# Performance work log

Hardware: AMD Instinct MI355X
Metric: run time of the kernel (lower is better)

## Reference

```python
import math
import jax, jax.numpy as jnp
import numpy as np

B, I, D, H, K, MAXI, FF = 2, 1024, 1024, 16, 64, 1024, 4096
DH = D // H
EPS = 1e-5

def _ln(x, g, b):
    m = x.mean(-1, keepdims=True)
    v = ((x - m) ** 2).mean(-1, keepdims=True)
    return (x - m) / jnp.sqrt(v + EPS) * g + b

def setup_inputs() -> dict:
    key = jax.random.key(0)
    ks = jax.random.split(key, 16)
    p = lambda i, sh: (0.02 * jax.random.normal(ks[i], sh)).astype(jnp.float32)
    # clamped relative-position indices: clamp(j - floor(1.0*i), -K, K) + K
    ar = np.arange(MAXI)
    idx = np.clip(ar[None, :] - ar[:, None], -K, K) + K  # [maxI, maxI]
    return {
        'x': jax.random.normal(ks[0], (B, I, D), dtype=jnp.float32),
        'j': jax.random.normal(ks[1], (B, I, D), dtype=jnp.float32),
        'ln1_g': jnp.ones((D,), jnp.float32), 'ln1_b': jnp.zeros((D,), jnp.float32),
        'Wv_w': p(2, (D, D)), 'Wv_b': jnp.zeros((D,), jnp.float32),
        'Wg_w': p(3, (D, D)), 'Wg_b': jnp.zeros((D,), jnp.float32),
        'lnv_g': jnp.ones((D,), jnp.float32), 'lnv_b': jnp.zeros((D,), jnp.float32),
        'Wq1_w': p(4, (D, D)), 'Wq1_b': jnp.zeros((D,), jnp.float32),
        'Wk_w': p(5, (D, D)), 'Wk_b': jnp.zeros((D,), jnp.float32),
        'Wq2_w': p(6, (D, D)), 'Wq2_b': jnp.zeros((D,), jnp.float32),
        'rel_emb': p(7, (2 * K + 1, D)),
        'Wo_w': p(8, (D, D)), 'Wo_b': jnp.zeros((D,), jnp.float32),
        'ln2_g': jnp.ones((D,), jnp.float32), 'ln2_b': jnp.zeros((D,), jnp.float32),
        'ff1_w': p(9, (D, FF)), 'ff1_b': jnp.zeros((FF,), jnp.float32),
        'ff2_w': p(10, (FF, D)), 'ff2_b': jnp.zeros((D,), jnp.float32),
        'indices': jnp.asarray(idx, jnp.int32),
    }

def reference(x, j, ln1_g, ln1_b, Wv_w, Wv_b, Wg_w, Wg_b, lnv_g, lnv_b,
              Wq1_w, Wq1_b, Wk_w, Wk_b, Wq2_w, Wq2_b, rel_emb,
              Wo_w, Wo_b, ln2_g, ln2_b, ff1_w, ff1_b, ff2_w, ff2_b, indices):
    Bv, Iq, _ = x.shape
    res = x
    xn = _ln(x, ln1_g, ln1_b)
    # value / gate streams with gelu activation, layernorm on v only
    v = _ln(jax.nn.gelu(xn @ Wv_w + Wv_b, approximate=False), lnv_g, lnv_b)
    g = jax.nn.gelu(xn @ Wg_w + Wg_b, approximate=False)
    vh = v.reshape(Bv, -1, H, DH)   # [B,J,H,Dh]
    gh = g.reshape(Bv, -1, H, DH)   # [B,I,H,Dh]
    # absolute-position scores: Q1(j) . K(j)^T
    q1 = (j @ Wq1_w + Wq1_b).reshape(Bv, -1, H, DH)
    kh = (j @ Wk_w + Wk_b).reshape(Bv, -1, H, DH)
    aa = jnp.einsum('bihd,bjhd->bhij', q1, kh)  # [B,H,I,J]
    # relative-position scores: Q2(j) . rel_embed^T, gathered by clamped indices
    q2 = (j @ Wq2_w + Wq2_b).reshape(Bv, -1, H, DH)
    rh = rel_emb.reshape(2 * K + 1, H, DH)
    arf = jnp.einsum('bihd,rhd->bhir', q2, rh)  # [B,H,I,2K+1]
    Jk = kh.shape[1]
    idx = jnp.broadcast_to(indices[None, None, :Iq, :Jk], (Bv, H, Iq, Jk))
    ar = jnp.take_along_axis(arf, idx, axis=-1)  # [B,H,I,J]
    a = jax.nn.softmax((aa + ar) / math.sqrt(DH), axis=-1)
    o = jnp.einsum('bhij,bjhd->bihd', a, vh) * gh  # gated attention output
    o = o.reshape(Bv, -1, D) @ Wo_w + Wo_b
    x1 = o + res
    # feed-forward sublayer
    h = jax.nn.relu(_ln(x1, ln2_g, ln2_b) @ ff1_w + ff1_b)
    out = h @ ff2_w + ff2_b + x1
    return (out, a)
```

## Files before the change

### kernel.cpp

```cpp
#include <hip/hip_runtime.h>
#include <hip/hip_bf16.h>
#include <math.h>

#define D_   1024
#define H_   16
#define DH_  64
#define FF_  4096
#define R_   129
#define I_   1024
#define B_   2
#define MROWS 2048
#define QKVLD 3072

typedef __bf16 v8bf16 __attribute__((ext_vector_type(8)));
typedef float f32x4 __attribute__((ext_vector_type(4)));

__device__ __forceinline__ float gelu_f(float x) {
    return 0.5f * x * (1.0f + erff(x * 0.7071067811865476f));
}

__device__ __forceinline__ void ldsld16(const void* g, void* l) {
    __builtin_amdgcn_global_load_lds(
        (const __attribute__((address_space(1))) void*)g,
        (__attribute__((address_space(3))) void*)l, 16, 0, 0);
}

__global__ __launch_bounds__(256) void cvt_bf16(const float* __restrict__ in,
        __hip_bfloat16* __restrict__ out, int n4) {
    int i = blockIdx.x * 256 + threadIdx.x;
    if (i >= n4) return;
    float4 v = reinterpret_cast<const float4*>(in)[i];
    union { __hip_bfloat16 h[4]; uint2 u; } pk;
    pk.h[0] = __float2bfloat16(v.x); pk.h[1] = __float2bfloat16(v.y);
    pk.h[2] = __float2bfloat16(v.z); pk.h[3] = __float2bfloat16(v.w);
    reinterpret_cast<uint2*>(out)[i] = pk.u;
}

__global__ __launch_bounds__(256) void wtrans(const float* __restrict__ W,
        __hip_bfloat16* __restrict__ WT, int K, int N) {
    __shared__ float T[64][65];
    int k0 = blockIdx.y * 64, n0 = blockIdx.x * 64;
    int t = threadIdx.x;
#pragma unroll
    for (int i = 0; i < 16; i++) {
        int e = t + i * 256, r = e >> 6, c = e & 63;
        T[r][c] = W[(size_t)(k0 + r) * N + n0 + c];
    }
    __syncthreads();
#pragma unroll
    for (int i = 0; i < 16; i++) {
        int e = t + i * 256, r = e >> 6, c = e & 63;
        WT[(size_t)(n0 + r) * K + k0 + c] = __float2bfloat16(T[c][r]);
    }
}

__global__ __launch_bounds__(256) void vtrans(const float* __restrict__ v,
        __hip_bfloat16* __restrict__ vt) {
    __shared__ float T[64][65];
    int z = blockIdx.y, b = z >> 4, h = z & 15;
    int j0 = blockIdx.x * 64;
    int t = threadIdx.x;
#pragma unroll
    for (int i = 0; i < 16; i++) {
        int e = t + i * 256, r = e >> 6, c = e & 63;
        T[r][c] = v[(size_t)(b * I_ + j0 + r) * D_ + h * DH_ + c];
    }
    __syncthreads();
#pragma unroll
    for (int i = 0; i < 16; i++) {
        int e = t + i * 256, r = e >> 6, c = e & 63;
        vt[((size_t)z * DH_ + r) * I_ + j0 + c] = __float2bfloat16(T[c][r]);
    }
}

template<int MR, int NWC, int ACT, int RES, int OUTBF>
__global__ __launch_bounds__(256) void gemm_mfma(
        const __hip_bfloat16* __restrict__ A,
        const __hip_bfloat16* __restrict__ Bt,
        const float* __restrict__ bias,
        const float* __restrict__ res,
        void* __restrict__ Cout,
        int N, int Kd, int lda, int ldb, int ldc,
        size_t sAb, size_t sAh, size_t sBb, size_t sBh, size_t sCz) {
    constexpr int NWR = 4 / NWC;
    constexpr int BM = NWR * MR * 16;
    constexpr int BN = NWC * 64;
    __shared__ __align__(16) __hip_bfloat16 As[BM * 64];
    __shared__ __align__(16) __hip_bfloat16 Bs[BN * 64];
    const char* AsB = (const char*)As;
    const char* BsB = (const char*)Bs;
    int z = blockIdx.z;
    const __hip_bfloat16* Ab = A + (size_t)(z >> 4) * sAb + (size_t)(z & 15) * sAh;
    const __hip_bfloat16* Bb = Bt + (size_t)(z >> 4) * sBb + (size_t)(z & 15) * sBh;
    float* Cf = (float*)Cout + (size_t)z * sCz;
    __hip_bfloat16* Cb = (__hip_bfloat16*)Cout + (size_t)z * sCz;
    int m0 = blockIdx.y * BM, n0 = blockIdx.x * BN;
    int t = threadIdx.x;
    int l = t & 63, w = t >> 6;
    int wr = w / NWC, wc = w % NWC;
    int lr = l & 15, kq = l >> 4;
    int rx = lr & 7;

    f32x4 acc[MR][4] = {};

    for (int k0 = 0; k0 < Kd; k0 += 64) {
#pragma unroll
        for (int i = 0; i < BM / 32; i++) {
            int e = t + i * 256;
            int row = e >> 3, sl = e & 7;
            int kb = sl ^ (row & 7);
            ldsld16(Ab + (size_t)(m0 + row) * lda + (k0 + kb * 8), (void*)(AsB + e * 16));
        }
#pragma unroll
        for (int i = 0; i < BN / 32; i++) {
            int e = t + i * 256;
            int row = e >> 3, sl = e & 7;
            int kb = sl ^ (row & 7);
            int nr = n0 + row; if (nr > N - 1) nr = N - 1;
            ldsld16(Bb + (size_t)nr * ldb + (k0 + kb * 8), (void*)(BsB + e * 16));
        }
        __syncthreads();
#pragma unroll
        for (int kc = 0; kc < 2; kc++) {
            int sloff = (((kc << 2) + kq) ^ rx) << 4;
            v8bf16 af[MR], bfr[4];
#pragma unroll
            for (int mr = 0; mr < MR; mr++)
                af[mr] = *(const v8bf16*)(AsB + ((wr * (MR * 16) + mr * 16 + lr) << 7) + sloff);
#pragma unroll
            for (int nc = 0; nc < 4; nc++)
                bfr[nc] = *(const v8bf16*)(BsB + ((wc * 64 + nc * 16 + lr) << 7) + sloff);
#pragma unroll
            for (int mr = 0; mr < MR; mr++)
#pragma unroll
                for (int nc = 0; nc < 4; nc++)
                    acc[mr][nc] = __builtin_amdgcn_mfma_f32_16x16x32_bf16(
                        af[mr], bfr[nc], acc[mr][nc], 0, 0, 0);
        }
        __syncthreads();
    }

#pragma unroll
    for (int mr = 0; mr < MR; mr++) {
        int rbase = m0 + wr * (MR * 16) + mr * 16 + kq * 4;
#pragma unroll
        for (int nc = 0; nc < 4; nc++) {
            int col = n0 + wc * 64 + nc * 16 + lr;
            bool okc = col < N;
            float bv = (bias && okc) ? bias[col] : 0.f;
#pragma unroll
            for (int ri = 0; ri < 4; ri++) {
                int r = rbase + ri;
                float val = acc[mr][nc][ri] + bv;
                if (ACT == 1) val = gelu_f(val);
                if (ACT == 2) val = fmaxf(val, 0.f);
                if (RES) val += res[(size_t)r * ldc + col];
                if (okc) {
                    if (OUTBF) Cb[(size_t)r * ldc + col] = __float2bfloat16(val);
                    else       Cf[(size_t)r * ldc + col] = val;
                }
            }
        }
    }
}

#define FA_AR 0
#define FA_K  16896
#define FA_V  (16896 + 8192)
#define FA_P  (16896 + 16384)
#define SC2   0.1803368801111244f
__global__ __launch_bounds__(256) void flash_attn3(
        const __hip_bfloat16* __restrict__ qkv,
        const __hip_bfloat16* __restrict__ vt,
        const __hip_bfloat16* __restrict__ arfb,
        const __hip_bfloat16* __restrict__ gb,
        float* __restrict__ a_out,
        __hip_bfloat16* __restrict__ obuf) {
    __shared__ __align__(16) char lds[16896 + 8192 * 3];
    __hip_bfloat16* arl = (__hip_bfloat16*)(lds + FA_AR);
    char* kB = lds + FA_K;
    char* vB = lds + FA_V;
    char* pB = lds + FA_P;

    int z = blockIdx.y, b = z >> 4, h = z & 15;
    int i0 = blockIdx.x * 64;
    int t = threadIdx.x, l = t & 63, w = t >> 6;
    int lr = l & 15, kq = l >> 4;

#pragma unroll
    for (int i = 0; i < 2; i++) {
        int e = t + i * 256;
        int row = e >> 3, sl = e & 7;
        int kb = sl ^ (row & 7);
        ldsld16(qkv + (size_t)(b * I_ + i0 + row) * QKVLD + h * DH_ + kb * 8,
                (void*)(pB + e * 16));
    }
    for (int idx = t; idx < 64 * 132; idx += 256) {
        int row = idx / 132, r = idx - row * 132;
        if (r < R_) arl[idx] = arfb[((size_t)z * I_ + i0 + row) * R_ + r];
    }
    __syncthreads();
    v8bf16 qf[2];
#pragma unroll
    for (int kc = 0; kc < 2; kc++)
        qf[kc] = *(const v8bf16*)(pB + ((w * 16 + lr) << 7) + ((((kc << 2) + kq) ^ (lr & 7)) << 4));

    int irow = w * 16 + kq * 4;
    int ig = i0 + irow;
    float loS[4], hiS[4];
#pragma unroll
    for (int ri = 0; ri < 4; ri++) {
        loS[ri] = __bfloat162float(arl[(irow + ri) * 132 + 0])   * SC2;
        hiS[ri] = __bfloat162float(arl[(irow + ri) * 132 + 128]) * SC2;
    }

    float l_ln[4] = {0.f, 0.f, 0.f, 0.f};
    for (int jt = 0; jt < 16; jt++) {
        int j0 = jt * 64;
#pragma unroll
        for (int i = 0; i < 2; i++) {
            int e = t + i * 256;
            int row = e >> 3, sl = e & 7;
            int kb = sl ^ (row & 7);
            ldsld16(qkv + (size_t)(b * I_ + j0 + row) * QKVLD + D_ + h * DH_ + kb * 8,
                    (void*)(kB + e * 16));
        }
        __syncthreads();
        f32x4 acc[4] = {};
#pragma unroll
        for (int kc = 0; kc < 2; kc++) {
            int sloff = ((((kc << 2) + kq)) ^ (lr & 7)) << 4;
#pragma unroll
            for (int tt = 0; tt < 4; tt++) {
                v8bf16 kf = *(const v8bf16*)(kB + ((tt * 16 + lr) << 7) + sloff);
                acc[tt] = __builtin_amdgcn_mfma_f32_16x16x32_bf16(qf[kc], kf, acc[tt], 0, 0, 0);
            }
        }
#pragma unroll
        for (int ri = 0; ri < 4; ri++) {
            int i_g = ig + ri;
            float sc[4];
            bool lo_all = (j0 + 63) <= (i_g - 64);
            bool hi_all = j0 >= (i_g + 64);
            if (lo_all || hi_all) {
                float c = lo_all ? loS[ri] : hiS[ri];
#pragma unroll
                for (int tt = 0; tt < 4; tt++) sc[tt] = fmaf(acc[tt][ri], SC2, c);
            } else {
#pragma unroll
                for (int tt = 0; tt < 4; tt++) {
                    int rel = j0 + tt * 16 + lr - i_g;
                    rel = rel < -64 ? -64 : (rel > 64 ? 64 : rel);
                    sc[tt] = (acc[tt][ri] + __bfloat162float(arl[(irow + ri) * 132 + rel + 64])) * SC2;
                }
            }
            l_ln[ri] += exp2f(sc[0]) + exp2f(sc[1]) + exp2f(sc[2]) + exp2f(sc[3]);
        }
        __syncthreads();
    }
    float offb[4];
#pragma unroll
    for (int ri = 0; ri < 4; ri++) {
        float s = l_ln[ri];
#pragma unroll
        for (int off = 1; off < 16; off <<= 1) s += __shfl_xor(s, off, 64);
        offb[ri] = __log2f(s);
    }

    f32x4 oacc[4] = {};
    for (int jt = 0; jt < 16; jt++) {
        int j0 = jt * 64;
#pragma unroll
        for (int i = 0; i < 2; i++) {
            int e = t + i * 256;
            int row = e >> 3, sl = e & 7;
            int kb = sl ^ (row & 7);
            ldsld16(qkv + (size_t)(b * I_ + j0 + row) * QKVLD + D_ + h * DH_ + kb * 8,
                    (void*)(kB + e * 16));
            ldsld16(vt + ((size_t)z * DH_ + row) * I_ + j0 + kb * 8,
                    (void*)(vB + e * 16));
        }
        __syncthreads();
        f32x4 acc[4] = {};
#pragma unroll
        for (int kc = 0; kc < 2; kc++) {
            int sloff = ((((kc << 2) + kq)) ^ (lr & 7)) << 4;
#pragma unroll
            for (int tt = 0; tt < 4; tt++) {
                v8bf16 kf = *(const v8bf16*)(kB + ((tt * 16 + lr) << 7) + sloff);
                acc[tt] = __builtin_amdgcn_mfma_f32_16x16x32_bf16(qf[kc], kf, acc[tt], 0, 0, 0);
            }
        }
#pragma unroll
        for (int ri = 0; ri < 4; ri++) {
            int i_g = ig + ri;
            int rowl = irow + ri;
            float sc[4];
            bool lo_all = (j0 + 63) <= (i_g - 64);
            bool hi_all = j0 >= (i_g + 64);
            if (lo_all || hi_all) {
                float c = lo_all ? loS[ri] : hiS[ri];
#pragma unroll
                for (int tt = 0; tt < 4; tt++) sc[tt] = fmaf(acc[tt][ri], SC2, c);
            } else {
#pragma unroll
                for (int tt = 0; tt < 4; tt++) {
                    int rel = j0 + tt * 16 + lr - i_g;
                    rel = rel < -64 ? -64 : (rel > 64 ? 64 : rel);
                    sc[tt] = (acc[tt][ri] + __bfloat162float(arl[rowl * 132 + rel + 64])) * SC2;
                }
            }
            float* gout = a_out + ((size_t)z * I_ + i0 + rowl) * I_ + j0;
#pragma unroll
            for (int tt = 0; tt < 4; tt++) {
                float p = exp2f(sc[tt] - offb[ri]);
                gout[tt * 16 + lr] = p;
                *(__hip_bfloat16*)(pB + (rowl << 7) +
                        ((((tt * 2) + (lr >> 3)) ^ (rowl & 7)) << 4) + (lr & 7) * 2) =
                    __float2bfloat16(p);
            }
        }
        __syncthreads();
#pragma unroll
        for (int kc = 0; kc < 2; kc++) {
            int sloff = ((((kc << 2) + kq)) ^ (lr & 7)) << 4;
            v8bf16 pf = *(const v8bf16*)(pB + ((w * 16 + lr) << 7) + sloff);
#pragma unroll
            for (int nc = 0; nc < 4; nc++) {
                v8bf16 vf = *(const v8bf16*)(vB + ((nc * 16 + lr) << 7) + sloff);
                oacc[nc] = __builtin_amdgcn_mfma_f32_16x16x32_bf16(pf, vf, oacc[nc], 0, 0, 0);
            }
        }
        __syncthreads();
    }
#pragma unroll
    for (int nc = 0; nc < 4; nc++) {
#pragma unroll
        for (int ri = 0; ri < 4; ri++) {
            int r = i0 + irow + ri;
            size_t oi = ((size_t)(b * I_ + r)) * D_ + h * DH_ + nc * 16 + lr;
            obuf[oi] = __float2bfloat16(oacc[nc][ri] * __bfloat162float(gb[oi]));
        }
    }
}

template<int OUTBF>
__global__ __launch_bounds__(256) void ln_kernel(const float* __restrict__ in,
        void* __restrict__ out, const float* __restrict__ gw,
        const float* __restrict__ bw) {
    __shared__ float shs[4], shq[4];
    int row = blockIdx.x;
    int t = threadIdx.x;
    float4 v = reinterpret_cast<const float4*>(in + (size_t)row * D_)[t];
    float s = v.x + v.y + v.z + v.w;
#pragma unroll
    for (int off = 32; off > 0; off >>= 1) s += __shfl_down(s, off, 64);
    if ((t & 63) == 0) shs[t >> 6] = s;
    __syncthreads();
    float mean = (shs[0] + shs[1] + shs[2] + shs[3]) * (1.0f / D_);
    float d0 = v.x - mean, d1 = v.y - mean, d2 = v.z - mean, d3 = v.w - mean;
    float q = d0 * d0 + d1 * d1 + d2 * d2 + d3 * d3;
#pragma unroll
    for (int off = 32; off > 0; off >>= 1) q += __shfl_down(q, off, 64);
    if ((t & 63) == 0) shq[t >> 6] = q;
    __syncthreads();
    float var = (shq[0] + shq[1] + shq[2] + shq[3]) * (1.0f / D_);
    float rstd = rsqrtf(var + 1e-5f);
    float4 g4 = reinterpret_cast<const float4*>(gw)[t];
    float4 b4 = reinterpret_cast<const float4*>(bw)[t];
    float o0 = d0 * rstd * g4.x + b4.x;
    float o1 = d1 * rstd * g4.y + b4.y;
    float o2 = d2 * rstd * g4.z + b4.z;
    float o3 = d3 * rstd * g4.w + b4.w;
    if (OUTBF) {
        union { __hip_bfloat16 h[4]; uint2 u; } pk;
        pk.h[0] = __float2bfloat16(o0); pk.h[1] = __float2bfloat16(o1);
        pk.h[2] = __float2bfloat16(o2); pk.h[3] = __float2bfloat16(o3);
        reinterpret_cast<uint2*>((__hip_bfloat16*)out + (size_t)row * D_)[t] = pk.u;
    } else {
        float4 o; o.x = o0; o.y = o1; o.z = o2; o.w = o3;
        reinterpret_cast<float4*>((float*)out + (size_t)row * D_)[t] = o;
    }
}

extern "C" void kernel_launch(void* const* d_in, const int* in_sizes, int n_in,
                              void* d_out, int out_size, void* d_ws, size_t ws_size,
                              hipStream_t stream) {
    const float* x      = (const float*)d_in[0];
    const float* jin    = (const float*)d_in[1];
    const float* ln1_g  = (const float*)d_in[2];
    const float* ln1_b  = (const float*)d_in[3];
    const float* Wv_w   = (const float*)d_in[4];
    const float* Wv_b   = (const float*)d_in[5];
    const float* Wg_w   = (const float*)d_in[6];
    const float* Wg_b   = (const float*)d_in[7];
    const float* lnv_g  = (const float*)d_in[8];
    const float* lnv_b  = (const float*)d_in[9];
    const float* Wq1_w  = (const float*)d_in[10];
    const float* Wq1_b  = (const float*)d_in[11];
    const float* Wk_w   = (const float*)d_in[12];
    const float* Wk_b   = (const float*)d_in[13];
    const float* Wq2_w  = (const float*)d_in[14];
    const float* Wq2_b  = (const float*)d_in[15];
    const float* rel    = (const float*)d_in[16];
    const float* Wo_w   = (const float*)d_in[17];
    const float* Wo_b   = (const float*)d_in[18];
    const float* ln2_g  = (const float*)d_in[19];
    const float* ln2_b  = (const float*)d_in[20];
    const float* ff1_w  = (const float*)d_in[21];
    const float* ff1_b  = (const float*)d_in[22];
    const float* ff2_w  = (const float*)d_in[23];
    const float* ff2_b  = (const float*)d_in[24];

    float* out0  = (float*)d_out;
    float* a_out = out0 + (size_t)B_ * I_ * D_;

    char* wsb = (char*)d_ws;
    const size_t MB = 1u << 20;
    __hip_bfloat16* WvT  = (__hip_bfloat16*)(wsb + 0 * MB);
    __hip_bfloat16* WgT  = (__hip_bfloat16*)(wsb + 2 * MB);
    __hip_bfloat16* qkvT = (__hip_bfloat16*)(wsb + 4 * MB);
    __hip_bfloat16* WoT  = (__hip_bfloat16*)(wsb + 10 * MB);
    __hip_bfloat16* ff1T = (__hip_bfloat16*)(wsb + 12 * MB);
    __hip_bfloat16* ff2T = (__hip_bfloat16*)(wsb + 20 * MB);
    __hip_bfloat16* jbf  = (__hip_bfloat16*)(wsb + 28 * MB);
    __hip_bfloat16* qkv  = (__hip_bfloat16*)(wsb + 32 * MB);
    __hip_bfloat16* relb = (__hip_bfloat16*)(wsb + 44 * MB);
    __hip_bfloat16* arfb = (__hip_bfloat16*)(wsb + 45 * MB);
    __hip_bfloat16* gbuf = (__hip_bfloat16*)(wsb + 54 * MB);
    float*          vbuf = (float*)        (wsb + 58 * MB);
    __hip_bfloat16* xnb  = (__hip_bfloat16*)(wsb + 28 * MB);
    __hip_bfloat16* vt   = (__hip_bfloat16*)(wsb + 28 * MB);
    __hip_bfloat16* obuf = (__hip_bfloat16*)(wsb + 58 * MB);
    float*          x1   = (float*)        (wsb + 32 * MB);
    __hip_bfloat16* x1nb = (__hip_bfloat16*)(wsb + 40 * MB);
    __hip_bfloat16* hbuf = (__hip_bfloat16*)(wsb + 44 * MB);
    float*          bias3= (float*)        (wsb + 66 * MB);

    dim3 blk(256);

    cvt_bf16<<<2048, blk, 0, stream>>>(jin, jbf, (MROWS * D_) / 4);
    cvt_bf16<<<129, blk, 0, stream>>>(rel, relb, (R_ * D_) / 4);
    hipMemcpyAsync(bias3,        Wq1_b, D_ * 4, hipMemcpyDeviceToDevice, stream);
    hipMemcpyAsync(bias3 + D_,   Wk_b,  D_ * 4, hipMemcpyDeviceToDevice, stream);
    hipMemcpyAsync(bias3 + 2*D_, Wq2_b, D_ * 4, hipMemcpyDeviceToDevice, stream);
    wtrans<<<dim3(16, 16), blk, 0, stream>>>(Wv_w, WvT, D_, D_);
    wtrans<<<dim3(16, 16), blk, 0, stream>>>(Wg_w, WgT, D_, D_);
    wtrans<<<dim3(16, 16), blk, 0, stream>>>(Wq1_w, qkvT,             D_, D_);
    wtrans<<<dim3(16, 16), blk, 0, stream>>>(Wk_w,  qkvT + 1024*1024, D_, D_);
    wtrans<<<dim3(16, 16), blk, 0, stream>>>(Wq2_w, qkvT + 2048*1024, D_, D_);
    wtrans<<<dim3(16, 16), blk, 0, stream>>>(Wo_w, WoT, D_, D_);
    wtrans<<<dim3(64, 16), blk, 0, stream>>>(ff1_w, ff1T, D_, FF_);
    wtrans<<<dim3(16, 64), blk, 0, stream>>>(ff2_w, ff2T, FF_, D_);

    gemm_mfma<2, 2, 0, 0, 1><<<dim3(24, 32, 1), blk, 0, stream>>>(
        jbf, qkvT, bias3, nullptr, qkv, QKVLD, D_, D_, D_, QKVLD, 0, 0, 0, 0, 0);
    gemm_mfma<4, 2, 0, 0, 1><<<dim3(2, 8, 32), blk, 0, stream>>>(
        qkv + 2 * D_, relb, nullptr, nullptr, arfb,
        R_, DH_, QKVLD, D_, R_,
        (size_t)I_ * QKVLD, (size_t)DH_, 0, (size_t)DH_, (size_t)I_ * R_);

    ln_kernel<1><<<MROWS, blk, 0, stream>>>(x, xnb, ln1_g, ln1_b);
    gemm_mfma<2, 1, 1, 0, 0><<<dim3(16, 16, 1), blk, 0, stream>>>(
        xnb, WvT, Wv_b, nullptr, vbuf, D_, D_, D_, D_, D_, 0, 0, 0, 0, 0);
    ln_kernel<0><<<MROWS, blk, 0, stream>>>(vbuf, vbuf, lnv_g, lnv_b);
    gemm_mfma<2, 1, 1, 0, 1><<<dim3(16, 16, 1), blk, 0, stream>>>(
        xnb, WgT, Wg_b, nullptr, gbuf, D_, D_, D_, D_, D_, 0, 0, 0, 0, 0);
    vtrans<<<dim3(16, 32), blk, 0, stream>>>(vbuf, vt);

    flash_attn3<<<dim3(16, 32), blk, 0, stream>>>(qkv, vt, arfb, gbuf, a_out, obuf);

    gemm_mfma<2, 1, 0, 1, 0><<<dim3(16, 16, 1), blk, 0, stream>>>(
        obuf, WoT, Wo_b, x, x1, D_, D_, D_, D_, D_, 0, 0, 0, 0, 0);
    ln_kernel<1><<<MROWS, blk, 0, stream>>>(x1, x1nb, ln2_g, ln2_b);
    gemm_mfma<4, 2, 2, 0, 1><<<dim3(32, 16, 1), blk, 0, stream>>>(
        x1nb, ff1T, ff1_b, nullptr, hbuf, FF_, D_, D_, D_, FF_, 0, 0, 0, 0, 0);
    gemm_mfma<2, 1, 0, 1, 0><<<dim3(16, 16, 1), blk, 0, stream>>>(
        hbuf, ff2T, ff2_b, x1, out0, D_, FF_, FF_, FF_, D_, 0, 0, 0, 0, 0);
}
```

Before: 311.2 us.

## Batch weight transposes, fuse Wv/Wg GEMMs, add MFMA priority and nontemporal stores

Six square weight transposes are merged into one launch using a z-indexed grid. The Wv and Wg projections become a single GEMM over concatenated transposed weights, with a new output mode that writes fp32 v and bf16 g to separate buffers. In flash attention, s_setprio raises wave priority around the MFMA blocks, and the large fp32 attention-probability writes become nontemporal stores. Together these cut launch count and redundant reads of xn, and reduce cache pollution, at the cost of more template branching and reusing the res pointer as a bf16 output. The combined GEMM passes ldc=D_ while N=2*D_, so the split store must index correctly, and that is a correctness risk.

```diff
diff --git a/kernel.cpp b/kernel.cpp
--- a/kernel.cpp
+++ b/kernel.cpp
@@ -51,6 +51,32 @@
     for (int i = 0; i < 16; i++) {
         int e = t + i * 256, r = e >> 6, c = e & 63;
         WT[(size_t)(n0 + r) * K + k0 + c] = __float2bfloat16(T[c][r]);
+    }
+}
+
+__global__ __launch_bounds__(256) void wtrans6(
+        const float* __restrict__ s0, const float* __restrict__ s1,
+        const float* __restrict__ s2, const float* __restrict__ s3,
+        const float* __restrict__ s4, const float* __restrict__ s5,
+        __hip_bfloat16* __restrict__ d0, __hip_bfloat16* __restrict__ d1,
+        __hip_bfloat16* __restrict__ d2, __hip_bfloat16* __restrict__ d3,
+        __hip_bfloat16* __restrict__ d4, __hip_bfloat16* __restrict__ d5) {
+    __shared__ float T[64][65];
+    int z = blockIdx.z;
+    const float* W = z == 0 ? s0 : z == 1 ? s1 : z == 2 ? s2 : z == 3 ? s3 : z == 4 ? s4 : s5;
+    __hip_bfloat16* WT = z == 0 ? d0 : z == 1 ? d1 : z == 2 ? d2 : z == 3 ? d3 : z == 4 ? d4 : d5;
+    int k0 = blockIdx.y * 64, n0 = blockIdx.x * 64;
+    int t = threadIdx.x;
+#pragma unroll
+    for (int i = 0; i < 16; i++) {
+        int e = t + i * 256, r = e >> 6, c = e & 63;
+        T[r][c] = W[(size_t)(k0 + r) * D_ + n0 + c];
+    }
+    __syncthreads();
+#pragma unroll
+    for (int i = 0; i < 16; i++) {
+        int e = t + i * 256, r = e >> 6, c = e & 63;
+        WT[(size_t)(n0 + r) * D_ + k0 + c] = __float2bfloat16(T[c][r]);
     }
 }
 
@@ -156,8 +182,15 @@
                 if (ACT == 2) val = fmaxf(val, 0.f);
                 if (RES) val += res[(size_t)r * ldc + col];
                 if (okc) {
-                    if (OUTBF) Cb[(size_t)r * ldc + col] = __float2bfloat16(val);
-                    else       Cf[(size_t)r * ldc + col] = val;
+                    if (OUTBF == 2) {
+                        if (col < D_) Cf[(size_t)r * ldc + col] = val;
+                        else ((__hip_bfloat16*)res)[(size_t)r * ldc + (col - D_)] =
+                                 __float2bfloat16(val);
+                    } else if (OUTBF == 1) {
+                        Cb[(size_t)r * ldc + col] = __float2bfloat16(val);
+                    } else {
+                        Cf[(size_t)r * ldc + col] = val;
+                    }
                 }
             }
         }
@@ -227,6 +260,7 @@
         }
         __syncthreads();
         f32x4 acc[4] = {};
+        __builtin_amdgcn_s_setprio(1);
 #pragma unroll
         for (int kc = 0; kc < 2; kc++) {
             int sloff = ((((kc << 2) + kq)) ^ (lr & 7)) << 4;
@@ -236,6 +270,7 @@
                 acc[tt] = __builtin_amdgcn_mfma_f32_16x16x32_bf16(qf[kc], kf, acc[tt], 0, 0, 0);
             }
         }
+        __builtin_amdgcn_s_setprio(0);
 #pragma unroll
         for (int ri = 0; ri < 4; ri++) {
             int i_g = ig + ri;
@@ -282,6 +317,7 @@
         }
         __syncthreads();
         f32x4 acc[4] = {};
+        __builtin_amdgcn_s_setprio(1);
 #pragma unroll
         for (int kc = 0; kc < 2; kc++) {
             int sloff = ((((kc << 2) + kq)) ^ (lr & 7)) << 4;
@@ -291,6 +327,7 @@
                 acc[tt] = __builtin_amdgcn_mfma_f32_16x16x32_bf16(qf[kc], kf, acc[tt], 0, 0, 0);
             }
         }
+        __builtin_amdgcn_s_setprio(0);
 #pragma unroll
         for (int ri = 0; ri < 4; ri++) {
             int i_g = ig + ri;
@@ -314,13 +351,14 @@
 #pragma unroll
             for (int tt = 0; tt < 4; tt++) {
                 float p = exp2f(sc[tt] - offb[ri]);
-                gout[tt * 16 + lr] = p;
+                __builtin_nontemporal_store(p, gout + tt * 16 + lr);
                 *(__hip_bfloat16*)(pB + (rowl << 7) +
                         ((((tt * 2) + (lr >> 3)) ^ (rowl & 7)) << 4) + (lr & 7) * 2) =
                     __float2bfloat16(p);
             }
         }
         __syncthreads();
+        __builtin_amdgcn_s_setprio(1);
 #pragma unroll
         for (int kc = 0; kc < 2; kc++) {
             int sloff = ((((kc << 2) + kq)) ^ (lr & 7)) << 4;
@@ -331,6 +369,7 @@
                 oacc[nc] = __builtin_amdgcn_mfma_f32_16x16x32_bf16(pf, vf, oacc[nc], 0, 0, 0);
             }
         }
+        __builtin_amdgcn_s_setprio(0);
         __syncthreads();
     }
 #pragma unroll
@@ -417,8 +456,7 @@
 
     char* wsb = (char*)d_ws;
     const size_t MB = 1u << 20;
-    __hip_bfloat16* WvT  = (__hip_bfloat16*)(wsb + 0 * MB);
-    __hip_bfloat16* WgT  = (__hip_bfloat16*)(wsb + 2 * MB);
+    __hip_bfloat16* wvwgT= (__hip_bfloat16*)(wsb + 0 * MB);
     __hip_bfloat16* qkvT = (__hip_bfloat16*)(wsb + 4 * MB);
     __hip_bfloat16* WoT  = (__hip_bfloat16*)(wsb + 10 * MB);
     __hip_bfloat16* ff1T = (__hip_bfloat16*)(wsb + 12 * MB);
@@ -436,6 +474,7 @@
     __hip_bfloat16* x1nb = (__hip_bfloat16*)(wsb + 40 * MB);
     __hip_bfloat16* hbuf = (__hip_bfloat16*)(wsb + 44 * MB);
     float*          bias3= (float*)        (wsb + 66 * MB);
+    float*          bias2= (float*)        (wsb + 66 * MB + 16384);
 
     dim3 blk(256);
 
@@ -444,12 +483,12 @@
     hipMemcpyAsync(bias3,        Wq1_b, D_ * 4, hipMemcpyDeviceToDevice, stream);
     hipMemcpyAsync(bias3 + D_,   Wk_b,  D_ * 4, hipMemcpyDeviceToDevice, stream);
     hipMemcpyAsync(bias3 + 2*D_, Wq2_b, D_ * 4, hipMemcpyDeviceToDevice, stream);
-    wtrans<<<dim3(16, 16), blk, 0, stream>>>(Wv_w, WvT, D_, D_);
-    wtrans<<<dim3(16, 16), blk, 0, stream>>>(Wg_w, WgT, D_, D_);
-    wtrans<<<dim3(16, 16), blk, 0, stream>>>(Wq1_w, qkvT,             D_, D_);
-    wtrans<<<dim3(16, 16), blk, 0, stream>>>(Wk_w,  qkvT + 1024*1024, D_, D_);
-    wtrans<<<dim3(16, 16), blk, 0, stream>>>(Wq2_w, qkvT + 2048*1024, D_, D_);
-    wtrans<<<dim3(16, 16), blk, 0, stream>>>(Wo_w, WoT, D_, D_);
+    hipMemcpyAsync(bias2,        Wv_b,  D_ * 4, hipMemcpyDeviceToDevice, stream);
+    hipMemcpyAsync(bias2 + D_,   Wg_b,  D_ * 4, hipMemcpyDeviceToDevice, stream);
+    wtrans6<<<dim3(16, 16, 6), blk, 0, stream>>>(
+        Wq1_w, Wk_w, Wq2_w, Wv_w, Wg_w, Wo_w,
+        qkvT, qkvT + 1024*1024, qkvT + 2048*1024,
+        wvwgT, wvwgT + 1024*1024, WoT);
     wtrans<<<dim3(64, 16), blk, 0, stream>>>(ff1_w, ff1T, D_, FF_);
     wtrans<<<dim3(16, 64), blk, 0, stream>>>(ff2_w, ff2T, FF_, D_);
 
@@ -461,11 +500,9 @@
         (size_t)I_ * QKVLD, (size_t)DH_, 0, (size_t)DH_, (size_t)I_ * R_);
 
     ln_kernel<1><<<MROWS, blk, 0, stream>>>(x, xnb, ln1_g, ln1_b);
-    gemm_mfma<2, 1, 1, 0, 0><<<dim3(16, 16, 1), blk, 0, stream>>>(
-        xnb, WvT, Wv_b, nullptr, vbuf, D_, D_, D_, D_, D_, 0, 0, 0, 0, 0);
+    gemm_mfma<2, 2, 1, 0, 2><<<dim3(16, 32, 1), blk, 0, stream>>>(
+        xnb, wvwgT, bias2, (const float*)gbuf, vbuf, 2 * D_, D_, D_, D_, D_, 0, 0, 0, 0, 0);
     ln_kernel<0><<<MROWS, blk, 0, stream>>>(vbuf, vbuf, lnv_g, lnv_b);
-    gemm_mfma<2, 1, 1, 0, 1><<<dim3(16, 16, 1), blk, 0, stream>>>(
-        xnb, WgT, Wg_b, nullptr, gbuf, D_, D_, D_, D_, D_, 0, 0, 0, 0, 0);
     vtrans<<<dim3(16, 32), blk, 0, stream>>>(vbuf, vt);
 
     flash_attn3<<<dim3(16, 32), blk, 0, stream>>>(qkv, vt, arfb, gbuf, a_out, obuf);
```

Measured after the change: 281.1 us. 9.7% less time.
